# Performance work log

Measured on AMD Instinct MI355X. Metric: run time of the kernel, lower is better.

## Reference

```python
import jax, jax.numpy as jnp
import numpy as np
import math

N, S, T, D = 4, 2048, 2048, 1024

def setup_inputs() -> dict:
    key = jax.random.key(0)
    ks = jax.random.split(key, 6)
    scale = 1.0 / math.sqrt(D)
    return {
        "query": jax.random.normal(ks[0], (N, S, D), dtype=jnp.float32),
        "key": jax.random.normal(ks[1], (N, T, D), dtype=jnp.float32),
        "value": jax.random.normal(ks[2], (N, T, D), dtype=jnp.float32),
        # causal mask: 1 = attend, 0 = masked out (masked_fill where mask == 0)
        "attn_mask": jnp.tril(jnp.ones((S, T), dtype=jnp.int32)),
        "Wq": jax.random.normal(ks[3], (D, D), dtype=jnp.float32) * scale,
        "Wk": jax.random.normal(ks[4], (D, D), dtype=jnp.float32) * scale,
        "Wv": jax.random.normal(ks[5], (D, D), dtype=jnp.float32) * scale,
    }

def reference(query, key, value, attn_mask, Wq, Wk, Wv):
    # nn.Linear(bias=False): y = x @ W.T
    q = jnp.einsum('nsd,ed->nse', query, Wq)
    k = jnp.einsum('ntd,ed->nte', key, Wk)
    v = jnp.einsum('ntd,ed->nte', value, Wv)
    # scaled dot-product scores [N, S, T]
    dot = jnp.einsum('nse,nte->nst', q, k) / jnp.sqrt(jnp.asarray(D, q.dtype))
    dot = jnp.where(attn_mask == 0, -jnp.inf, dot)
    scores = jax.nn.softmax(dot, axis=-1)
    # dropout is identity in eval mode
    y = jnp.einsum('nst,nte->nse', scores, v)
    return y
```

## Files before the change

kernel.cpp:

```cpp
#include <hip/hip_runtime.h>
#include <math.h>

using u16 = unsigned short;
typedef __attribute__((ext_vector_type(8))) __bf16 bf16x8;
typedef __attribute__((ext_vector_type(4))) float f32x4;
typedef __attribute__((ext_vector_type(4))) float f4v;
typedef __attribute__((ext_vector_type(8))) u16 u16x8;

__device__ __forceinline__ u16 f2bf(float f) {
  unsigned u = __float_as_uint(f);
  u += 0x7fffu + ((u >> 16) & 1u);
  return (u16)(u >> 16);
}
__device__ __forceinline__ float bf2f(u16 b) {
  unsigned u = ((unsigned)b) << 16;
  return __uint_as_float(u);
}

__device__ __forceinline__ void gload16(const void* g, void* l) {
  __builtin_amdgcn_global_load_lds(
      (const __attribute__((address_space(1))) unsigned int*)g,
      (__attribute__((address_space(3))) unsigned int*)l, 16, 0, 0);
}

__device__ __forceinline__ f32x4 MF(bf16x8 a, bf16x8 b, f32x4 c) {
  return __builtin_amdgcn_mfma_f32_16x16x32_bf16(a, b, c, 0, 0, 0);
}

__global__ __launch_bounds__(256) void cast3_f32_bf16(
    const float* __restrict__ p0, const float* __restrict__ p1,
    const float* __restrict__ p2, u16* __restrict__ out, size_t ostride) {
  int z = blockIdx.z;
  const float* in = (z == 0) ? p0 : (z == 1) ? p1 : p2;
  size_t i = ((size_t)blockIdx.x * 256 + threadIdx.x) * 8;
  f4v a = *reinterpret_cast<const f4v*>(in + i);
  f4v b = *reinterpret_cast<const f4v*>(in + i + 4);
  u16x8 r;
  r[0] = f2bf(a[0]); r[1] = f2bf(a[1]); r[2] = f2bf(a[2]); r[3] = f2bf(a[3]);
  r[4] = f2bf(b[0]); r[5] = f2bf(b[1]); r[6] = f2bf(b[2]); r[7] = f2bf(b[3]);
  *reinterpret_cast<u16x8*>(out + z * ostride + i) = r;
}

__global__ __launch_bounds__(256) void wprep(
    const float* __restrict__ Wk, const float* __restrict__ Wq,
    const float* __restrict__ Wv, u16* __restrict__ wkT,
    u16* __restrict__ wqT, u16* __restrict__ wv_bf) {
  int z = blockIdx.z;
  if (z < 2) {
    __shared__ float t[64][65];
    const float* I = z ? Wq : Wk;
    u16* O = z ? wqT : wkT;
    int c0 = blockIdx.x * 64, r0 = blockIdx.y * 64;
    int tx = threadIdx.x & 63, ty = threadIdx.x >> 6;
    #pragma unroll
    for (int i = 0; i < 64; i += 4)
      t[ty + i][tx] = I[(size_t)(r0 + ty + i) * 1024 + c0 + tx];
    __syncthreads();
    #pragma unroll
    for (int i = 0; i < 64; i += 4)
      O[(size_t)(c0 + ty + i) * 1024 + r0 + tx] = f2bf(t[tx][ty + i]);
  } else {
    int b = blockIdx.y * 16 + blockIdx.x;
    size_t i = (size_t)b * 4096 + threadIdx.x * 16;
    #pragma unroll
    for (int h = 0; h < 2; ++h) {
      f4v a = *reinterpret_cast<const f4v*>(Wv + i + h * 8);
      f4v c = *reinterpret_cast<const f4v*>(Wv + i + h * 8 + 4);
      u16x8 r;
      r[0] = f2bf(a[0]); r[1] = f2bf(a[1]); r[2] = f2bf(a[2]); r[3] = f2bf(a[3]);
      r[4] = f2bf(c[0]); r[5] = f2bf(c[1]); r[6] = f2bf(c[2]); r[7] = f2bf(c[3]);
      *reinterpret_cast<u16x8*>(wv_bf + i + h * 8) = r;
    }
  }
}

template<typename OutT, int MODE>
__global__ __launch_bounds__(512) void gemm_bt8(
    const u16* __restrict__ A, const u16* __restrict__ B, OutT* __restrict__ C,
    int K, int lda, int ldb, int ldc,
    size_t sA, size_t sB, size_t sC, float alpha,
    OutT* __restrict__ C1) {
  int bn, bm, bz = 0;
  int kEnd = K;
  bool whichV = false;
  const u16 *Ag, *Bg;
  OutT* Cg;
  if (MODE == 0) {
    bm = blockIdx.x >> 3;
    bn = blockIdx.x & 7;
    Ag = A + (size_t)bm * 128 * lda;
    Bg = B + (size_t)bn * 128 * ldb;
    Cg = C;
  } else if (MODE == 1) {
    int h = blockIdx.x;
    int l = (h & 7) * 68 + (h >> 3);
    bz = l / 136;
    int t = l % 136;
    bm = (int)((sqrtf(8.f * (float)t + 1.f) - 1.f) * 0.5f);
    while ((bm + 1) * (bm + 2) / 2 <= t) ++bm;
    while (bm * (bm + 1) / 2 > t) --bm;
    bn = t - bm * (bm + 1) / 2;
    Ag = A + sA * bz + (size_t)bm * 128 * lda;
    Bg = B + sB * bz + (size_t)bn * 128 * ldb;
    Cg = C + sC * bz;
  } else if (MODE == 2) {
    int l = blockIdx.x;
    bm = 15 - (l >> 5);
    int rest = l & 31;
    bz = rest >> 3;
    bn = rest & 7;
    kEnd = (K < (bm + 1) * 128) ? K : (bm + 1) * 128;
    Ag = A + sA * bz + (size_t)bm * 128 * lda;
    Bg = B + sB * bz + (size_t)bn * 128 * ldb;
    Cg = C + sC * bz;
  } else {
    int h = blockIdx.x;
    int l = (h & 7) * 128 + (h >> 3);
    bn = l & 7;
    int bm128 = l >> 3;
    whichV = (bm128 >> 6) != 0;
    bm = bm128 & 63;
    Ag = A + (size_t)bm128 * 128 * lda;
    Bg = B + (whichV ? sB : 0) + (size_t)bn * 128 * ldb;
    Cg = C;
  }

  __shared__ __align__(16) char smem[33024];
  u16* AsB = (u16*)smem;
  u16* BsB = AsB + 8192;

  const int tid = threadIdx.x;
  const int lane = tid & 63, wv = tid >> 6;
  const int wr = wv >> 2, wc = wv & 3;
  const int fr = lane & 15, kq = (lane >> 4) * 8;

  const int e0 = wv * 512 + lane * 8;
  const int r0 = e0 >> 5, c0 = e0 & 31;
  const u16* a0 = Ag + (size_t)r0 * lda + c0;
  const u16* b0 = Bg + (size_t)r0 * ldb + c0;

  f32x4 acc[4][2] = {};
  const int nt = kEnd / 32;

  gload16(a0, &AsB[wv * 512]);
  gload16(b0, &BsB[wv * 512]);
  __syncthreads();

  for (int t = 0; t < nt; ++t) {
    const int cur = t & 1;
    if (t + 1 < nt) {
      const int k0 = (t + 1) * 32;
      gload16(a0 + k0, &AsB[(cur ^ 1) * 4096 + wv * 512]);
      gload16(b0 + k0, &BsB[(cur ^ 1) * 4096 + wv * 512]);
    }
    const u16* Ac = AsB + cur * 4096;
    const u16* Bc = BsB + cur * 4096;
    bf16x8 af[4], bfv[2];
    #pragma unroll
    for (int m = 0; m < 4; ++m)
      af[m] = *reinterpret_cast<const bf16x8*>(&Ac[(wr * 64 + m * 16 + fr) * 32 + kq]);
    #pragma unroll
    for (int n = 0; n < 2; ++n)
      bfv[n] = *reinterpret_cast<const bf16x8*>(&Bc[(wc * 32 + n * 16 + fr) * 32 + kq]);
    #pragma unroll
    for (int m = 0; m < 4; ++m)
      #pragma unroll
      for (int n = 0; n < 2; ++n)
        acc[m][n] = MF(af[m], bfv[n], acc[m][n]);
    __syncthreads();
  }

  if constexpr (MODE == 3) {
    if (whichV) {
      u16* tt = (u16*)smem;
      #pragma unroll
      for (int m = 0; m < 4; ++m)
        #pragma unroll
        for (int n = 0; n < 2; ++n)
          #pragma unroll
          for (int j = 0; j < 4; ++j)
            tt[(wr * 64 + (lane >> 4) * 4 + m * 16 + j) * 129 +
               (wc * 32 + fr + n * 16)] = f2bf(acc[m][n][j]);
      __syncthreads();
      const int orow = tid >> 2, oc = (tid & 3) * 32;
      size_t base = (size_t)(bm >> 4) * (1024 * 2048) +
                    (size_t)(bn * 128 + orow) * 2048 +
                    (size_t)(bm & 15) * 128 + oc;
      #pragma unroll
      for (int jj = 0; jj < 4; ++jj) {
        u16x8 o;
        #pragma unroll
        for (int j = 0; j < 8; ++j) o[j] = tt[(oc + jj * 8 + j) * 129 + orow];
        *reinterpret_cast<u16x8*>(&C1[base + jj * 8]) = o;
      }
      return;
    }
  }

  const int row0 = bm * 128 + wr * 64 + (lane >> 4) * 4;
  const int col0 = bn * 128 + wc * 32 + fr;
  #pragma unroll
  for (int m = 0; m < 4; ++m)
    #pragma unroll
    for (int n = 0; n < 2; ++n) {
      #pragma unroll
      for (int j = 0; j < 4; ++j) {
        float val = acc[m][n][j] * alpha;
        size_t idx = (size_t)(row0 + m * 16 + j) * ldc + (col0 + n * 16);
        if constexpr (sizeof(OutT) == 2) Cg[idx] = f2bf(val);
        else Cg[idx] = val;
      }
    }
}

__global__ __launch_bounds__(256) void softmax_causal(u16* __restrict__ sc) {
  int r = blockIdx.x;
  int s = r & 2047;
  u16* row = sc + (size_t)r * 2048;
  int tid = threadIdx.x;
  int t0 = tid * 8;
  u16x8 raw = {0, 0, 0, 0, 0, 0, 0, 0};
  if (t0 <= s) raw = *reinterpret_cast<const u16x8*>(row + t0);
  float v[8];
  float mx = -1e30f;
  #pragma unroll
  for (int j = 0; j < 8; ++j) {
    v[j] = ((t0 + j) <= s) ? bf2f(raw[j]) : -1e30f;
    mx = fmaxf(mx, v[j]);
  }
  #pragma unroll
  for (int o = 32; o; o >>= 1) mx = fmaxf(mx, __shfl_xor(mx, o, 64));
  __shared__ float red[8];
  if ((tid & 63) == 0) red[tid >> 6] = mx;
  __syncthreads();
  mx = fmaxf(fmaxf(red[0], red[1]), fmaxf(red[2], red[3]));
  float p[8];
  float sum = 0.f;
  #pragma unroll
  for (int j = 0; j < 8; ++j) {
    p[j] = ((t0 + j) <= s) ? __expf(v[j] - mx) : 0.f;
    sum += p[j];
  }
  #pragma unroll
  for (int o = 32; o; o >>= 1) sum += __shfl_xor(sum, o, 64);
  if ((tid & 63) == 0) red[4 + (tid >> 6)] = sum;
  __syncthreads();
  sum = red[4] + red[5] + red[6] + red[7];
  float inv = 1.0f / sum;
  u16x8 o8;
  #pragma unroll
  for (int j = 0; j < 8; ++j) o8[j] = f2bf(p[j] * inv);
  if (t0 <= (s | 127))
    *reinterpret_cast<u16x8*>(row + t0) = o8;
}

extern "C" void kernel_launch(void* const* d_in, const int* in_sizes, int n_in,
                              void* d_out, int out_size, void* d_ws, size_t ws_size,
                              hipStream_t stream) {
  const float* q  = (const float*)d_in[0];
  const float* k  = (const float*)d_in[1];
  const float* v  = (const float*)d_in[2];
  const float* Wq = (const float*)d_in[4];
  const float* Wk = (const float*)d_in[5];
  const float* Wv = (const float*)d_in[6];
  float* out = (float*)d_out;
  char* ws = (char*)d_ws;

  const size_t MB = 1024ull * 1024ull;
  u16* sc   = (u16*)ws;
  u16* qb   = (u16*)ws;
  u16* xk   = (u16*)(ws + 32 * MB);
  u16* wsl  = (u16*)(ws + 48 * MB);
  u16* wkT  = (u16*)(ws + 52 * MB);
  u16* wqT  = (u16*)(ws + 54 * MB);
  u16* Vt   = (u16*)(ws + 56 * MB);
  u16* Yq   = (u16*)(ws + 72 * MB);
  (void)in_sizes; (void)n_in; (void)out_size; (void)ws_size;

  wprep<<<dim3(16, 16, 3), 256, 0, stream>>>(Wk, Wq, Wv, wkT, wqT,
                                             wsl + 1048576);

  gemm_bt8<u16, 0><<<64, 512, 0, stream>>>(
      wkT, wqT, wsl, 1024, 1024, 1024, 1024, 0, 0, 0, 1.0f, nullptr);

  cast3_f32_bf16<<<dim3(4096, 1, 3), 256, 0, stream>>>(q, v, k, qb, 8ull * MB);

  gemm_bt8<u16, 3><<<1024, 512, 0, stream>>>(
      qb, wsl, Yq, 1024, 1024, 1024, 1024,
      0, 1048576, 0, 1.0f, Vt);

  gemm_bt8<u16, 1><<<544, 512, 0, stream>>>(
      Yq, xk, sc, 1024, 1024, 1024, 2048,
      (size_t)2048 * 1024, (size_t)2048 * 1024, (size_t)2048 * 2048, 0.03125f,
      nullptr);

  softmax_causal<<<8192, 256, 0, stream>>>(sc);

  gemm_bt8<float, 2><<<512, 512, 0, stream>>>(
      sc, Vt, out, 2048, 2048, 2048, 1024,
      (size_t)2048 * 2048, (size_t)1024 * 2048, (size_t)2048 * 1024, 1.0f,
      nullptr);
}
```

Measured before the change: 170.8 us.

## Fuse causal softmax into score GEMM epilogue and PV GEMM operand load

Removes the standalone softmax kernel. The score GEMM now writes masked, scaled bf16 logits (masked entries set to -100) and accumulates per-row sums of exp(logit) into a float buffer with atomics. That buffer is zeroed in the weight-prep kernel. The PV GEMM exponentiates the A fragments on load and divides by the row sum in its epilogue. This saves a full read and write pass over the score matrix and one launch, but drops max subtraction, so it relies on logits staying small enough not to overflow. It also recomputes exp redundantly across the waves that share rows.

```diff
diff --git a/kernel.cpp b/kernel.cpp
--- a/kernel.cpp
+++ b/kernel.cpp
@@ -25,6 +25,13 @@
 
 __device__ __forceinline__ f32x4 MF(bf16x8 a, bf16x8 b, f32x4 c) {
   return __builtin_amdgcn_mfma_f32_16x16x32_bf16(a, b, c, 0, 0, 0);
+}
+
+__device__ __forceinline__ bf16x8 expb(bf16x8 a) {
+  bf16x8 r;
+  #pragma unroll
+  for (int j = 0; j < 8; ++j) r[j] = (__bf16)__expf((float)a[j]);
+  return r;
 }
 
 __global__ __launch_bounds__(256) void cast3_f32_bf16(
@@ -44,7 +51,7 @@
 __global__ __launch_bounds__(256) void wprep(
     const float* __restrict__ Wk, const float* __restrict__ Wq,
     const float* __restrict__ Wv, u16* __restrict__ wkT,
-    u16* __restrict__ wqT, u16* __restrict__ wv_bf) {
+    u16* __restrict__ wqT, u16* __restrict__ wv_bf, float* __restrict__ lbuf) {
   int z = blockIdx.z;
   if (z < 2) {
     __shared__ float t[64][65];
@@ -59,7 +66,7 @@
     #pragma unroll
     for (int i = 0; i < 64; i += 4)
       O[(size_t)(c0 + ty + i) * 1024 + r0 + tx] = f2bf(t[tx][ty + i]);
-  } else {
+  } else if (z == 2) {
     int b = blockIdx.y * 16 + blockIdx.x;
     size_t i = (size_t)b * 4096 + threadIdx.x * 16;
     #pragma unroll
@@ -71,6 +78,10 @@
       r[4] = f2bf(c[0]); r[5] = f2bf(c[1]); r[6] = f2bf(c[2]); r[7] = f2bf(c[3]);
       *reinterpret_cast<u16x8*>(wv_bf + i + h * 8) = r;
     }
+  } else {
+    if (blockIdx.y) return;
+    int i = blockIdx.x * 512 + threadIdx.x * 2;
+    if (i < 8192) { lbuf[i] = 0.f; lbuf[i + 1] = 0.f; }
   }
 }
 
@@ -79,7 +90,7 @@
     const u16* __restrict__ A, const u16* __restrict__ B, OutT* __restrict__ C,
     int K, int lda, int ldb, int ldc,
     size_t sA, size_t sB, size_t sC, float alpha,
-    OutT* __restrict__ C1) {
+    OutT* __restrict__ C1, float* __restrict__ lbuf) {
   int bn, bm, bz = 0;
   int kEnd = K;
   bool whichV = false;
@@ -133,6 +144,7 @@
   const int lane = tid & 63, wv = tid >> 6;
   const int wr = wv >> 2, wc = wv & 3;
   const int fr = lane & 15, kq = (lane >> 4) * 8;
+  const int g4 = (lane >> 4) * 4;
 
   const int e0 = wv * 512 + lane * 8;
   const int r0 = e0 >> 5, c0 = e0 & 31;
@@ -157,8 +169,10 @@
     const u16* Bc = BsB + cur * 4096;
     bf16x8 af[4], bfv[2];
     #pragma unroll
-    for (int m = 0; m < 4; ++m)
+    for (int m = 0; m < 4; ++m) {
       af[m] = *reinterpret_cast<const bf16x8*>(&Ac[(wr * 64 + m * 16 + fr) * 32 + kq]);
+      if constexpr (MODE == 2) af[m] = expb(af[m]);
+    }
     #pragma unroll
     for (int n = 0; n < 2; ++n)
       bfv[n] = *reinterpret_cast<const bf16x8*>(&Bc[(wc * 32 + n * 16 + fr) * 32 + kq]);
@@ -170,6 +184,46 @@
     __syncthreads();
   }
 
+  if constexpr (MODE == 1) {
+    float psum[4][4];
+    #pragma unroll
+    for (int m = 0; m < 4; ++m)
+      #pragma unroll
+      for (int j = 0; j < 4; ++j) {
+        int tr = wr * 64 + g4 + m * 16 + j;
+        float rs = 0.f;
+        #pragma unroll
+        for (int n = 0; n < 2; ++n) {
+          float val = acc[m][n][j] * alpha;
+          int tc = wc * 32 + fr + n * 16;
+          if (bm == bn && tc > tr) val = -100.f;
+          Cg[(size_t)(bm * 128 + tr) * ldc + (bn * 128 + tc)] = f2bf(val);
+          rs += __expf(val);
+        }
+        psum[m][j] = rs;
+      }
+    #pragma unroll
+    for (int o = 1; o < 16; o <<= 1)
+      #pragma unroll
+      for (int m = 0; m < 4; ++m)
+        #pragma unroll
+        for (int j = 0; j < 4; ++j)
+          psum[m][j] += __shfl_xor(psum[m][j], o, 64);
+    float* lsum = (float*)smem;
+    if (fr == 0)
+      #pragma unroll
+      for (int m = 0; m < 4; ++m)
+        #pragma unroll
+        for (int j = 0; j < 4; ++j)
+          lsum[wc * 128 + wr * 64 + g4 + m * 16 + j] = psum[m][j];
+    __syncthreads();
+    if (tid < 128) {
+      float s = lsum[tid] + lsum[128 + tid] + lsum[256 + tid] + lsum[384 + tid];
+      atomicAdd(&lbuf[(size_t)bz * 2048 + bm * 128 + tid], s);
+    }
+    return;
+  }
+
   if constexpr (MODE == 3) {
     if (whichV) {
       u16* tt = (u16*)smem;
@@ -179,7 +233,7 @@
         for (int n = 0; n < 2; ++n)
           #pragma unroll
           for (int j = 0; j < 4; ++j)
-            tt[(wr * 64 + (lane >> 4) * 4 + m * 16 + j) * 129 +
+            tt[(wr * 64 + g4 + m * 16 + j) * 129 +
                (wc * 32 + fr + n * 16)] = f2bf(acc[m][n][j]);
       __syncthreads();
       const int orow = tid >> 2, oc = (tid & 3) * 32;
@@ -197,7 +251,16 @@
     }
   }
 
-  const int row0 = bm * 128 + wr * 64 + (lane >> 4) * 4;
+  float il[4][4];
+  if constexpr (MODE == 2) {
+    #pragma unroll
+    for (int m = 0; m < 4; ++m)
+      #pragma unroll
+      for (int j = 0; j < 4; ++j)
+        il[m][j] = 1.0f / lbuf[(size_t)bz * 2048 + bm * 128 + wr * 64 + g4 + m * 16 + j];
+  }
+
+  const int row0 = bm * 128 + wr * 64 + g4;
   const int col0 = bn * 128 + wc * 32 + fr;
   #pragma unroll
   for (int m = 0; m < 4; ++m)
@@ -206,52 +269,12 @@
       #pragma unroll
       for (int j = 0; j < 4; ++j) {
         float val = acc[m][n][j] * alpha;
+        if constexpr (MODE == 2) val = acc[m][n][j] * il[m][j];
         size_t idx = (size_t)(row0 + m * 16 + j) * ldc + (col0 + n * 16);
         if constexpr (sizeof(OutT) == 2) Cg[idx] = f2bf(val);
         else Cg[idx] = val;
       }
     }
-}
-
-__global__ __launch_bounds__(256) void softmax_causal(u16* __restrict__ sc) {
-  int r = blockIdx.x;
-  int s = r & 2047;
-  u16* row = sc + (size_t)r * 2048;
-  int tid = threadIdx.x;
-  int t0 = tid * 8;
-  u16x8 raw = {0, 0, 0, 0, 0, 0, 0, 0};
-  if (t0 <= s) raw = *reinterpret_cast<const u16x8*>(row + t0);
-  float v[8];
-  float mx = -1e30f;
-  #pragma unroll
-  for (int j = 0; j < 8; ++j) {
-    v[j] = ((t0 + j) <= s) ? bf2f(raw[j]) : -1e30f;
-    mx = fmaxf(mx, v[j]);
-  }
-  #pragma unroll
-  for (int o = 32; o; o >>= 1) mx = fmaxf(mx, __shfl_xor(mx, o, 64));
-  __shared__ float red[8];
-  if ((tid & 63) == 0) red[tid >> 6] = mx;
-  __syncthreads();
-  mx = fmaxf(fmaxf(red[0], red[1]), fmaxf(red[2], red[3]));
-  float p[8];
-  float sum = 0.f;
-  #pragma unroll
-  for (int j = 0; j < 8; ++j) {
-    p[j] = ((t0 + j) <= s) ? __expf(v[j] - mx) : 0.f;
-    sum += p[j];
-  }
-  #pragma unroll
-  for (int o = 32; o; o >>= 1) sum += __shfl_xor(sum, o, 64);
-  if ((tid & 63) == 0) red[4 + (tid >> 6)] = sum;
-  __syncthreads();
-  sum = red[4] + red[5] + red[6] + red[7];
-  float inv = 1.0f / sum;
-  u16x8 o8;
-  #pragma unroll
-  for (int j = 0; j < 8; ++j) o8[j] = f2bf(p[j] * inv);
-  if (t0 <= (s | 127))
-    *reinterpret_cast<u16x8*>(row + t0) = o8;
 }
 
 extern "C" void kernel_launch(void* const* d_in, const int* in_sizes, int n_in,
@@ -275,29 +298,28 @@
   u16* wqT  = (u16*)(ws + 54 * MB);
   u16* Vt   = (u16*)(ws + 56 * MB);
   u16* Yq   = (u16*)(ws + 72 * MB);
+  float* lb = (float*)(ws + 88 * MB);
   (void)in_sizes; (void)n_in; (void)out_size; (void)ws_size;
 
-  wprep<<<dim3(16, 16, 3), 256, 0, stream>>>(Wk, Wq, Wv, wkT, wqT,
-                                             wsl + 1048576);
+  wprep<<<dim3(16, 16, 4), 256, 0, stream>>>(Wk, Wq, Wv, wkT, wqT,
+                                             wsl + 1048576, lb);
 
   gemm_bt8<u16, 0><<<64, 512, 0, stream>>>(
-      wkT, wqT, wsl, 1024, 1024, 1024, 1024, 0, 0, 0, 1.0f, nullptr);
+      wkT, wqT, wsl, 1024, 1024, 1024, 1024, 0, 0, 0, 1.0f, nullptr, nullptr);
 
   cast3_f32_bf16<<<dim3(4096, 1, 3), 256, 0, stream>>>(q, v, k, qb, 8ull * MB);
 
   gemm_bt8<u16, 3><<<1024, 512, 0, stream>>>(
       qb, wsl, Yq, 1024, 1024, 1024, 1024,
-      0, 1048576, 0, 1.0f, Vt);
+      0, 1048576, 0, 1.0f, Vt, nullptr);
 
   gemm_bt8<u16, 1><<<544, 512, 0, stream>>>(
       Yq, xk, sc, 1024, 1024, 1024, 2048,
       (size_t)2048 * 1024, (size_t)2048 * 1024, (size_t)2048 * 2048, 0.03125f,
-      nullptr);
-
-  softmax_causal<<<8192, 256, 0, stream>>>(sc);
+      nullptr, lb);
 
   gemm_bt8<float, 2><<<512, 512, 0, stream>>>(
       sc, Vt, out, 2048, 2048, 2048, 1024,
       (size_t)2048 * 2048, (size_t)1024 * 2048, (size_t)2048 * 1024, 1.0f,
-      nullptr);
-}
+      nullptr, lb);
+}
```

New measurement: 191.6 us. 1.12x slower.
